# Optimization experiments

Measured on AMD Instinct MI355X. Metric: run time of the kernel, lower is better.

Reference implementation:

```python
import jax, jax.numpy as jnp
import numpy as np

B, T, C = 4, 2048, 1024   # batch, seq (block_size), n_embd
H, D = 16, 64             # num_heads, head_size (H*D == C)


def setup_inputs() -> dict:
    key = jax.random.key(0)
    ks = jax.random.split(key, 6)
    s = 0.02
    return {
        "x":  jax.random.normal(ks[0], (B, T, C), jnp.float32),
        "Wq": jax.random.normal(ks[1], (H, C, D), jnp.float32) * s,
        "Wk": jax.random.normal(ks[2], (H, C, D), jnp.float32) * s,
        "Wv": jax.random.normal(ks[3], (H, C, D), jnp.float32) * s,
        "Wp": jax.random.normal(ks[4], (C, C), jnp.float32) * s,
        "bp": jnp.zeros((C,), jnp.float32),
        "is_masked": 1,
    }


def reference(x, Wq, Wk, Wv, Wp, bp, is_masked):
    # Batched per-head projections (original loops over H separate Linears)
    q = jnp.einsum("btc,hcd->bhtd", x, Wq)
    k = jnp.einsum("btc,hcd->bhtd", x, Wk)
    v = jnp.einsum("btc,hcd->bhtd", x, Wv)
    # NOTE: original divides by sqrt(C) where C = n_embd (input dim), not head_size
    scores = jnp.einsum("bhtd,bhsd->bhts", q, k) / jnp.sqrt(jnp.asarray(C, x.dtype))
    if is_masked:
        causal = jnp.tril(jnp.ones((T, T), bool))
        scores = jnp.where(causal, scores, jnp.asarray(-jnp.inf, scores.dtype))
    attn = jax.nn.softmax(scores, axis=-1)   # dropout is identity in eval mode
    out = jnp.einsum("bhts,bhsd->bhtd", attn, v)
    # concat heads along the last dim: [B,T,H*D] == [B,T,C]
    out = out.transpose(0, 2, 1, 3).reshape(B, T, C)
    return out @ Wp.T + bp
```

## Files before the change

### kernel.cpp

```cpp
#include <hip/hip_runtime.h>
#include <stdint.h>
#include <type_traits>

typedef unsigned short u16;
typedef unsigned int u32;
typedef __attribute__((ext_vector_type(8))) short frag8;
typedef __attribute__((ext_vector_type(4))) float fx4;
typedef __attribute__((ext_vector_type(16))) float fx16;

#define MFMA(a, b, c) __builtin_amdgcn_mfma_f32_16x16x32_bf16((a), (b), (c), 0, 0, 0)
#define MFMA32(a, b, c) __builtin_amdgcn_mfma_f32_32x32x16_bf16((a), (b), (c), 0, 0, 0)

__device__ __forceinline__ void gload16(const void* g, void* l) {
  __builtin_amdgcn_global_load_lds((const __attribute__((address_space(1))) void*)g,
                                   (__attribute__((address_space(3))) void*)l, 16, 0, 0);
}

__device__ __forceinline__ u16 f2bf(float f) {
  union { float f; unsigned int u; } c; c.f = f;
  unsigned int r = c.u + 0x7FFFu + ((c.u >> 16) & 1u);
  return (u16)(r >> 16);
}

__device__ __forceinline__ u32 cvtpk(float lo, float hi) {
  u32 r;
  asm("v_cvt_pk_bf16_f32 %0, %1, %2" : "=v"(r) : "v"(lo), "v"(hi));
  return r;
}

__device__ __forceinline__ float fmax3(float a, float b, float c) {
  return fmaxf(fmaxf(a, b), c);
}


__global__ __launch_bounds__(256) void cvt_x(const float* __restrict__ x, u16* __restrict__ xb) {
  const int n4 = (8192 * 1024) / 4;
  for (int i = blockIdx.x * 256 + threadIdx.x; i < n4; i += 2048 * 256) {
    float4 v = ((const float4*)x)[i];
    ushort4 o;
    o.x = f2bf(v.x); o.y = f2bf(v.y); o.z = f2bf(v.z); o.w = f2bf(v.w);
    ((ushort4*)xb)[i] = o;
  }
}

__global__ __launch_bounds__(256) void cvt_wqkv(const float* __restrict__ Wq,
                                                const float* __restrict__ Wk,
                                                const float* __restrict__ Wv,
                                                u16* __restrict__ Wt) {
  __shared__ u16 Tls[64][72];
  int hh = blockIdx.x;
  int c0 = blockIdx.y * 64;
  int type = hh >> 4, h = hh & 15;
  const float* Wsrc = (type == 0 ? Wq : (type == 1 ? Wk : Wv)) + (size_t)h * 1024 * 64;
  int t = threadIdx.x;
  int cr = t >> 4, q4 = (t & 15) * 4;
  for (int i = 0; i < 4; ++i) {
    int c = cr + i * 16;
    float4 v = *(const float4*)(Wsrc + (size_t)(c0 + c) * 64 + q4);
    Tls[q4 + 0][c] = f2bf(v.x);
    Tls[q4 + 1][c] = f2bf(v.y);
    Tls[q4 + 2][c] = f2bf(v.z);
    Tls[q4 + 3][c] = f2bf(v.w);
  }
  __syncthreads();
  for (int i = 0; i < 4; ++i) {
    int d = cr + i * 16;
    ushort4 o;
    o.x = Tls[d][q4 + 0]; o.y = Tls[d][q4 + 1]; o.z = Tls[d][q4 + 2]; o.w = Tls[d][q4 + 3];
    *(ushort4*)(Wt + ((size_t)hh * 64 + d) * 1024 + c0 + q4) = o;
  }
}

__global__ __launch_bounds__(256) void cvt_wp(const float* __restrict__ Wp, u16* __restrict__ wb) {
  const int n4 = (1024 * 1024) / 4;
  for (int i = blockIdx.x * 256 + threadIdx.x; i < n4; i += 1024 * 256) {
    float4 v = ((const float4*)Wp)[i];
    ushort4 o;
    o.x = f2bf(v.x); o.y = f2bf(v.y); o.z = f2bf(v.z); o.w = f2bf(v.w);
    ((ushort4*)wb)[i] = o;
  }
}

__global__ __launch_bounds__(256) void transpose_v(const u16* __restrict__ Vb, u16* __restrict__ VTg) {
  __shared__ u16 T[64 * 64];
  int bh = blockIdx.x, t0 = blockIdx.y * 64;
  const u16* src = Vb + ((size_t)bh * 2048 + t0) * 64;
  int tid = threadIdx.x;
  int tl = tid >> 2, c16 = (tid & 3) * 16;
  int swzw = (tl & 7) << 4;
  frag8 a = *(const frag8*)(src + (size_t)tl * 64 + c16);
  frag8 b = *(const frag8*)(src + (size_t)tl * 64 + c16 + 8);
  *(frag8*)((char*)T + tl * 128 + ((c16 * 2) ^ swzw)) = a;
  *(frag8*)((char*)T + tl * 128 + ((c16 * 2 + 16) ^ swzw)) = b;
  __syncthreads();
  int d_ = tid & 63;
#pragma unroll
  for (int k = 0; k < 2; ++k) {
    int c_ = (tid >> 6) + 4 * k;
    frag8 o;
#pragma unroll
    for (int j = 0; j < 8; ++j) {
      int t = c_ * 8 + j;
      o[j] = *(const u16*)((const char*)T + t * 128 + ((2 * d_) ^ ((t & 7) << 4)));
    }
    *(frag8*)(VTg + ((size_t)bh * 64 + d_) * 2048 + t0 + c_ * 8) = o;
  }
}


template <int BN, int MODE>
__global__ __launch_bounds__(512, 1) void gemm2(const u16* __restrict__ A, const u16* __restrict__ Bw,
                                                u16* __restrict__ Qb, u16* __restrict__ Kb,
                                                u16* __restrict__ Vb, float* __restrict__ outp,
                                                const float* __restrict__ bp) {
  constexpr int NI = BN / 32;
  constexpr int NB = BN / 64;
  constexpr int BBYTES = BN * 128;
  __shared__ __align__(16) char LDSC[65536 + 3 * BBYTES];
  const int tid = threadIdx.x, w = tid >> 6, lane = tid & 63;
  const int lr = lane & 15, lg = lane >> 4;
  constexpr int NBY = (BN == 192) ? 16 : 8;
  const int wg = blockIdx.x;
  const int xcd = wg & 7, loc = wg >> 3;
  const int bx = xcd * 4 + loc / NBY;
  const int by = loc % NBY;
  const int m0 = bx * 256, n0 = by * BN;
  const int r8 = lane >> 3;
  const int c8 = ((lane & 7) ^ r8) * 8;
  const u16* aS[4];
  const u16* bS[3];
#pragma unroll
  for (int l = 0; l < 4; ++l) aS[l] = A + (size_t)(m0 + l * 64 + w * 8 + r8) * 1024 + c8;
#pragma unroll
  for (int l = 0; l < NB; ++l) bS[l] = Bw + (size_t)(n0 + l * 64 + w * 8 + r8) * 1024 + c8;
  const int wmB = (w >> 1) * 64, wnB = (w & 1) * (BN / 2);

  auto rdA = [&](const char* ab, int mi, int ks) -> frag8 {
    int row = wmB + mi * 16 + lr;
    return *(const frag8*)(ab + row * 128 + ((((ks << 2) + lg) ^ (lr & 7)) << 4));
  };
  auto rdB = [&](const char* bbuf, int ni, int ks) -> frag8 {
    int row = wnB + ni * 16 + lr;
    return *(const frag8*)(bbuf + row * 128 + ((((ks << 2) + lg) ^ (lr & 7)) << 4));
  };

  fx4 acc[4][NI] = {};

#pragma unroll
  for (int l = 0; l < 4; ++l) gload16(aS[l], LDSC + l * 8192 + w * 1024);
#pragma unroll
  for (int l = 0; l < NB; ++l) gload16(bS[l], LDSC + 65536 + l * 8192 + w * 1024);
#pragma unroll
  for (int l = 0; l < NB; ++l) gload16(bS[l] + 64, LDSC + 65536 + BBYTES + l * 8192 + w * 1024);
  if constexpr (NB == 3) asm volatile("s_waitcnt vmcnt(3)" ::: "memory");
  else asm volatile("s_waitcnt vmcnt(2)" ::: "memory");
  __builtin_amdgcn_s_barrier();

  for (int t = 0; t < 16; ++t) {
    const char* ab = LDSC + (t & 1) * 32768;
    const char* bb = LDSC + 65536 + (t % 3) * BBYTES;
    char* abN = LDSC + ((t + 1) & 1) * 32768;
    char* bbN = LDSC + 65536 + ((t + 2) % 3) * BBYTES;
    if (t + 1 < 16) {
#pragma unroll
      for (int l = 0; l < 4; ++l) gload16(aS[l] + (t + 1) * 64, abN + l * 8192 + w * 1024);
    }
    if (t + 2 < 16) {
#pragma unroll
      for (int l = 0; l < NB; ++l) gload16(bS[l] + (t + 2) * 64, bbN + l * 8192 + w * 1024);
    }
    frag8 Bf[NI][2];
#pragma unroll
    for (int ni = 0; ni < NI; ++ni) {
      Bf[ni][0] = rdB(bb, ni, 0);
      Bf[ni][1] = rdB(bb, ni, 1);
    }
    frag8 a0 = rdA(ab, 0, 0), a1 = rdA(ab, 0, 1);
#pragma unroll
    for (int mi = 0; mi < 4; ++mi) {
      frag8 c0 = a0, c1 = a1;
      if (mi < 3) {
        a0 = rdA(ab, mi + 1, 0);
        a1 = rdA(ab, mi + 1, 1);
      }
      __builtin_amdgcn_s_setprio(1);
#pragma unroll
      for (int ni = 0; ni < NI; ++ni) {
        acc[mi][ni] = MFMA(c0, Bf[ni][0], acc[mi][ni]);
        acc[mi][ni] = MFMA(c1, Bf[ni][1], acc[mi][ni]);
      }
      __builtin_amdgcn_s_setprio(0);
    }
    if (t < 14) {
      if constexpr (NB == 3) asm volatile("s_waitcnt vmcnt(3)" ::: "memory");
      else asm volatile("s_waitcnt vmcnt(2)" ::: "memory");
    } else {
      asm volatile("s_waitcnt vmcnt(0)" ::: "memory");
    }
    __builtin_amdgcn_s_barrier();
  }

#pragma unroll
  for (int mi = 0; mi < 4; ++mi)
#pragma unroll
    for (int r = 0; r < 4; ++r) {
      int m = m0 + wmB + mi * 16 + lg * 4 + r;
      if (MODE == 0) {
        int b = m >> 11, tt = m & 2047;
#pragma unroll
        for (int ni = 0; ni < NI; ++ni) {
          int n = n0 + wnB + ni * 16 + lr;
          int type = n >> 10, h = (n >> 6) & 15, d = n & 63;
          u16* dst = (type == 0) ? Qb : ((type == 1) ? Kb : Vb);
          float v = acc[mi][ni][r];
          if (type == 0) v *= 0.04508422002778011f;
          dst[((size_t)(b * 16 + h) * 2048 + tt) * 64 + d] = f2bf(v);
        }
      } else {
#pragma unroll
        for (int ni = 0; ni < NI; ++ni) {
          int n = n0 + wnB + ni * 16 + lr;
          outp[(size_t)m * 1024 + n] = acc[mi][ni][r] + bp[n];
        }
      }
    }
}


__global__ __launch_bounds__(256, 4) void attn(const u16* __restrict__ Qb, const u16* __restrict__ Kb,
                                               const u16* __restrict__ VTg, u16* __restrict__ Ao,
                                               const int* __restrict__ mflag) {
  __shared__ __align__(16) char LDS[32768];
  const int tid = threadIdx.x, w = tid >> 6, lane = tid & 63;
  const int l31 = lane & 31, hi = lane >> 5;
  const int bh = blockIdx.x;
  const int qt = 15 - (int)blockIdx.y;
  const int masked = mflag[0];
  const int qbase = qt * 128;
  const u16* Qh = Qb + (size_t)bh * (2048 * 64);
  const u16* Kh = Kb + (size_t)bh * (2048 * 64);
  const u16* Vh = VTg + (size_t)bh * (64 * 2048);
  const int qrow = qbase + w * 32 + l31;
  frag8 qf[4];
#pragma unroll
  for (int s = 0; s < 4; ++s) qf[s] = *(const frag8*)(Qh + (size_t)qrow * 64 + s * 16 + hi * 8);
  const int srow = lane >> 3;
  const int schunk = ((lane & 7) ^ srow) * 8;
  const int c0 = w * 2, c1 = w * 2 + 1;
  const u16* kg0 = Kh + (size_t)(c0 * 8 + srow) * 64 + schunk;
  const u16* kg1 = Kh + (size_t)(c1 * 8 + srow) * 64 + schunk;
  const u16* vg0 = Vh + (size_t)(c0 * 8 + srow) * 2048 + schunk;
  const u16* vg1 = Vh + (size_t)(c1 * 8 + srow) * 2048 + schunk;
  const int aK = l31 * 128 + ((hi * 16) ^ ((l31 & 7) << 4));
  const int qmax_w = qbase + w * 32 + 31;
  const int qmin_w = qbase + w * 32;
  float m_run = -__builtin_inff(), l_run = 0.f;
  fx16 oa0 = {}, oa1 = {};
  const int nt = masked ? (2 * qt + 2) : 32;

  auto STAGE = [&](int B, int T) {
    size_t ko = (size_t)T * 4096, vo = (size_t)T * 64;
    gload16(kg0 + ko, LDS + B * 8192 + c0 * 1024);
    gload16(kg1 + ko, LDS + B * 8192 + c1 * 1024);
    gload16(vg0 + vo, LDS + 16384 + B * 8192 + c0 * 1024);
    gload16(vg1 + vo, LDS + 16384 + B * 8192 + c1 * 1024);
  };

  auto TILE = [&](auto Bc, int T) {
    constexpr int B = decltype(Bc)::value;
    if (T + 1 < nt) STAGE(B ^ 1, T + 1);
    bool act = (!masked) || (T * 64 <= qmax_w);
    if (act) {
      fx16 s0v = {}, s1v = {};
#pragma unroll
      for (int ds = 0; ds < 4; ++ds) {
        frag8 k0 = *(const frag8*)(LDS + B * 8192 + (aK ^ (ds << 5)));
        frag8 k1 = *(const frag8*)(LDS + B * 8192 + 4096 + (aK ^ (ds << 5)));
        s0v = MFMA32(k0, qf[ds], s0v);
        s1v = MFMA32(k1, qf[ds], s1v);
      }
      if (masked && T * 64 + 63 > qmin_w) {
#pragma unroll
        for (int g = 0; g < 4; ++g)
#pragma unroll
          for (int r = 0; r < 4; ++r) {
            int sg = T * 64 + r + 8 * g + 4 * hi;
            if (sg > qrow) s0v[4 * g + r] = -__builtin_inff();
            if (sg + 32 > qrow) s1v[4 * g + r] = -__builtin_inff();
          }
      }
      float tmx[8];
#pragma unroll
      for (int i = 0; i < 8; ++i)
        tmx[i] = fmaxf(fmaxf(s0v[i], s0v[i + 8]), fmaxf(s1v[i], s1v[i + 8]));
      float r0 = fmax3(tmx[0], tmx[1], tmx[2]);
      float r1 = fmax3(tmx[3], tmx[4], tmx[5]);
      float r2 = fmax3(tmx[6], tmx[7], r0);
      float mx = fmaxf(r1, r2);
      mx = fmaxf(mx, __int_as_float(__shfl_xor(__float_as_int(mx), 32)));
      if (!__all(mx <= m_run + 8.0f)) {
        float mn = fmaxf(m_run, mx);
        float al = __builtin_amdgcn_exp2f(m_run - mn);
#pragma unroll
        for (int i = 0; i < 16; ++i) { oa0[i] *= al; oa1[i] *= al; }
        l_run *= al;
        m_run = mn;
      }
#pragma unroll
      for (int i = 0; i < 16; ++i) s0v[i] = __builtin_amdgcn_exp2f(s0v[i] - m_run);
#pragma unroll
      for (int i = 0; i < 16; ++i) s1v[i] = __builtin_amdgcn_exp2f(s1v[i] - m_run);
      float tps[8];
#pragma unroll
      for (int i = 0; i < 8; ++i)
        tps[i] = (s0v[i] + s0v[i + 8]) + (s1v[i] + s1v[i + 8]);
      float u0 = (tps[0] + tps[1]) + (tps[2] + tps[3]);
      float u1 = (tps[4] + tps[5]) + (tps[6] + tps[7]);
      float ps = u0 + u1;
      ps += __int_as_float(__shfl_xor(__float_as_int(ps), 32));
      l_run += ps;
#pragma unroll
      for (int kt = 0; kt < 4; ++kt) {
        const int b8 = (kt & 1) * 8;
        float p0, p1, p2, p3, p4, p5, p6, p7;
        if (kt < 2) { p0=s0v[b8+0];p1=s0v[b8+1];p2=s0v[b8+2];p3=s0v[b8+3];p4=s0v[b8+4];p5=s0v[b8+5];p6=s0v[b8+6];p7=s0v[b8+7]; }
        else        { p0=s1v[b8+0];p1=s1v[b8+1];p2=s1v[b8+2];p3=s1v[b8+3];p4=s1v[b8+4];p5=s1v[b8+5];p6=s1v[b8+6];p7=s1v[b8+7]; }
        u32 X0 = cvtpk(p0, p1), X1 = cvtpk(p2, p3);
        u32 Y0 = cvtpk(p4, p5), Y1 = cvtpk(p6, p7);
        u32 sel0 = hi ? X0 : Y0, sel1 = hi ? X1 : Y1;
        u32 got0 = (u32)__shfl_xor((int)sel0, 32);
        u32 got1 = (u32)__shfl_xor((int)sel1, 32);
        union { u32 u[4]; frag8 f; } pf;
        pf.u[0] = hi ? got0 : X0;
        pf.u[1] = hi ? got1 : X1;
        pf.u[2] = hi ? Y0 : got0;
        pf.u[3] = hi ? Y1 : got1;
        frag8 v0 = *(const frag8*)(LDS + 16384 + B * 8192 + (aK ^ (kt << 5)));
        frag8 v1 = *(const frag8*)(LDS + 16384 + B * 8192 + 4096 + (aK ^ (kt << 5)));
        oa0 = MFMA32(v0, pf.f, oa0);
        oa1 = MFMA32(v1, pf.f, oa1);
      }
    }
    asm volatile("s_waitcnt vmcnt(0)" ::: "memory");
    __builtin_amdgcn_s_barrier();
  };

  STAGE(0, 0);
  asm volatile("s_waitcnt vmcnt(0)" ::: "memory");
  __builtin_amdgcn_s_barrier();
  int t = 0;
  while (true) {
    TILE(std::integral_constant<int, 0>{}, t); ++t; if (t >= nt) break;
    TILE(std::integral_constant<int, 1>{}, t); ++t; if (t >= nt) break;
  }

  float inv = 1.0f / l_run;
  int b = bh >> 4, hh = bh & 15;
  u16* orow = Ao + ((size_t)b * 2048 + qrow) * 1024 + hh * 64;
#pragma unroll
  for (int g = 0; g < 4; ++g) {
    int d0 = 8 * g + 4 * hi;
    u32 wA = cvtpk(oa0[4 * g + 0] * inv, oa0[4 * g + 1] * inv);
    u32 wB = cvtpk(oa0[4 * g + 2] * inv, oa0[4 * g + 3] * inv);
    u32 wC = cvtpk(oa1[4 * g + 0] * inv, oa1[4 * g + 1] * inv);
    u32 wD = cvtpk(oa1[4 * g + 2] * inv, oa1[4 * g + 3] * inv);
    *(u32*)(orow + d0 + 0) = wA;
    *(u32*)(orow + d0 + 2) = wB;
    *(u32*)(orow + d0 + 32) = wC;
    *(u32*)(orow + d0 + 34) = wD;
  }
}


extern "C" void kernel_launch(void* const* d_in, const int* in_sizes, int n_in,
                              void* d_out, int out_size, void* d_ws, size_t ws_size,
                              hipStream_t stream) {
  const float* x = (const float*)d_in[0];
  const float* Wq = (const float*)d_in[1];
  const float* Wk = (const float*)d_in[2];
  const float* Wv = (const float*)d_in[3];
  const float* Wp = (const float*)d_in[4];
  const float* bp = (const float*)d_in[5];
  const int* is_masked = (const int*)d_in[6];
  float* out = (float*)d_out;
  char* ws = (char*)d_ws;
  u16* Xbf = (u16*)(ws + 0);
  u16* Wt  = (u16*)(ws + 16777216);
  u16* Wpb = (u16*)(ws + 23068672);
  u16* Qb  = (u16*)(ws + 25165824);
  u16* Kb  = (u16*)(ws + 41943040);
  u16* Vb  = (u16*)(ws + 58720256);
  u16* Ao  = (u16*)(ws + 75497472);
  u16* VTg = Xbf;

  cvt_x<<<2048, 256, 0, stream>>>(x, Xbf);
  cvt_wqkv<<<dim3(48, 16), 256, 0, stream>>>(Wq, Wk, Wv, Wt);
  cvt_wp<<<1024, 256, 0, stream>>>(Wp, Wpb);
  gemm2<192, 0><<<512, 512, 0, stream>>>(Xbf, Wt, Qb, Kb, Vb, nullptr, nullptr);
  transpose_v<<<dim3(64, 32), 256, 0, stream>>>(Vb, VTg);
  attn<<<dim3(64, 16), 256, 0, stream>>>(Qb, Kb, VTg, Ao, is_masked);
  gemm2<128, 1><<<256, 512, 0, stream>>>(Ao, Wpb, nullptr, nullptr, nullptr, out, bp);
}
```

Before: 162.4 us.

## Restructure GEMM mainloop into barrier-phased MFMA pairs and shrink attention query tiles

The GEMM mainloop now preloads all A fragments and computes output columns in pairs, with barrier-separated phases, explicit lgkmcnt waits and sched_barriers, and B-tile prefetches spread across the phases. Launch bounds are raised to two blocks per SM. The attention kernel moves from 128-row query tiles with 4 waves to 64-row tiles with 2 waves, doubling the grid and dropping the per-wave causal skip check. The aim is better load/MFMA interleaving and better causal load balance, at the cost of extra barriers and more K/V traffic per query row.

After: 174.1 us. 1.07x slower.

```diff
diff --git a/kernel.cpp b/kernel.cpp
--- a/kernel.cpp
+++ b/kernel.cpp
@@ -109,11 +109,12 @@
 
 
 template <int BN, int MODE>
-__global__ __launch_bounds__(512, 1) void gemm2(const u16* __restrict__ A, const u16* __restrict__ Bw,
+__global__ __launch_bounds__(512, 2) void gemm2(const u16* __restrict__ A, const u16* __restrict__ Bw,
                                                 u16* __restrict__ Qb, u16* __restrict__ Kb,
                                                 u16* __restrict__ Vb, float* __restrict__ outp,
                                                 const float* __restrict__ bp) {
   constexpr int NI = BN / 32;
+  constexpr int NPAIR = NI / 2;
   constexpr int NB = BN / 64;
   constexpr int BBYTES = BN * 128;
   __shared__ __align__(16) char LDSC[65536 + 3 * BBYTES];
@@ -156,48 +157,77 @@
   else asm volatile("s_waitcnt vmcnt(2)" ::: "memory");
   __builtin_amdgcn_s_barrier();
 
+  int bcur = 0;
   for (int t = 0; t < 16; ++t) {
     const char* ab = LDSC + (t & 1) * 32768;
-    const char* bb = LDSC + 65536 + (t % 3) * BBYTES;
+    const char* bb = LDSC + 65536 + bcur * BBYTES;
     char* abN = LDSC + ((t + 1) & 1) * 32768;
-    char* bbN = LDSC + 65536 + ((t + 2) % 3) * BBYTES;
+    int bn2 = bcur + 2; if (bn2 >= 3) bn2 -= 3;
+    char* bbN = LDSC + 65536 + bn2 * BBYTES;
+
+    frag8 Af[4][2];
+#pragma unroll
+    for (int mi = 0; mi < 4; ++mi) {
+      Af[mi][0] = rdA(ab, mi, 0);
+      Af[mi][1] = rdA(ab, mi, 1);
+    }
+    frag8 Bf[2][2];
+    Bf[0][0] = rdB(bb, 0, 0); Bf[0][1] = rdB(bb, 0, 1);
+    Bf[1][0] = rdB(bb, 1, 0); Bf[1][1] = rdB(bb, 1, 1);
     if (t + 1 < 16) {
 #pragma unroll
       for (int l = 0; l < 4; ++l) gload16(aS[l] + (t + 1) * 64, abN + l * 8192 + w * 1024);
     }
-    if (t + 2 < 16) {
-#pragma unroll
-      for (int l = 0; l < NB; ++l) gload16(bS[l] + (t + 2) * 64, bbN + l * 8192 + w * 1024);
-    }
-    frag8 Bf[NI][2];
-#pragma unroll
-    for (int ni = 0; ni < NI; ++ni) {
-      Bf[ni][0] = rdB(bb, ni, 0);
-      Bf[ni][1] = rdB(bb, ni, 1);
-    }
-    frag8 a0 = rdA(ab, 0, 0), a1 = rdA(ab, 0, 1);
-#pragma unroll
-    for (int mi = 0; mi < 4; ++mi) {
-      frag8 c0 = a0, c1 = a1;
-      if (mi < 3) {
-        a0 = rdA(ab, mi + 1, 0);
-        a1 = rdA(ab, mi + 1, 1);
-      }
+    __builtin_amdgcn_s_barrier();
+    asm volatile("s_waitcnt lgkmcnt(0)" ::: "memory");
+    __builtin_amdgcn_sched_barrier(0);
+    __builtin_amdgcn_s_setprio(1);
+#pragma unroll
+    for (int mi = 0; mi < 4; ++mi)
+#pragma unroll
+      for (int ks = 0; ks < 2; ++ks) {
+        acc[mi][0] = MFMA(Af[mi][ks], Bf[0][ks], acc[mi][0]);
+        acc[mi][1] = MFMA(Af[mi][ks], Bf[1][ks], acc[mi][1]);
+      }
+    __builtin_amdgcn_s_setprio(0);
+    __builtin_amdgcn_s_barrier();
+
+#pragma unroll
+    for (int p = 1; p < NPAIR; ++p) {
+      frag8 Bp[2][2];
+      Bp[0][0] = rdB(bb, 2 * p + 0, 0); Bp[0][1] = rdB(bb, 2 * p + 0, 1);
+      Bp[1][0] = rdB(bb, 2 * p + 1, 0); Bp[1][1] = rdB(bb, 2 * p + 1, 1);
+      if (t + 2 < 16) {
+        if (p == 1) {
+          gload16(bS[0] + (t + 2) * 64, bbN + 0 * 8192 + w * 1024);
+          if (NB > 2 || NPAIR == 2) gload16(bS[1] + (t + 2) * 64, bbN + 1 * 8192 + w * 1024);
+        }
+        if (NPAIR == 3 && p == 2 && NB == 3)
+          gload16(bS[2] + (t + 2) * 64, bbN + 2 * 8192 + w * 1024);
+      }
+      __builtin_amdgcn_s_barrier();
+      asm volatile("s_waitcnt lgkmcnt(0)" ::: "memory");
+      __builtin_amdgcn_sched_barrier(0);
       __builtin_amdgcn_s_setprio(1);
 #pragma unroll
-      for (int ni = 0; ni < NI; ++ni) {
-        acc[mi][ni] = MFMA(c0, Bf[ni][0], acc[mi][ni]);
-        acc[mi][ni] = MFMA(c1, Bf[ni][1], acc[mi][ni]);
-      }
+      for (int mi = 0; mi < 4; ++mi)
+#pragma unroll
+        for (int ks = 0; ks < 2; ++ks) {
+          acc[mi][2 * p + 0] = MFMA(Af[mi][ks], Bp[0][ks], acc[mi][2 * p + 0]);
+          acc[mi][2 * p + 1] = MFMA(Af[mi][ks], Bp[1][ks], acc[mi][2 * p + 1]);
+        }
       __builtin_amdgcn_s_setprio(0);
-    }
-    if (t < 14) {
-      if constexpr (NB == 3) asm volatile("s_waitcnt vmcnt(3)" ::: "memory");
-      else asm volatile("s_waitcnt vmcnt(2)" ::: "memory");
-    } else {
-      asm volatile("s_waitcnt vmcnt(0)" ::: "memory");
-    }
-    __builtin_amdgcn_s_barrier();
+      if (p == NPAIR - 1) {
+        if (t < 14) {
+          if constexpr (NB == 3) asm volatile("s_waitcnt vmcnt(3)" ::: "memory");
+          else asm volatile("s_waitcnt vmcnt(2)" ::: "memory");
+        } else {
+          asm volatile("s_waitcnt vmcnt(0)" ::: "memory");
+        }
+      }
+      __builtin_amdgcn_s_barrier();
+    }
+    bcur += 1; if (bcur == 3) bcur = 0;
   }
 
 #pragma unroll
@@ -227,16 +257,16 @@
 }
 
 
-__global__ __launch_bounds__(256, 4) void attn(const u16* __restrict__ Qb, const u16* __restrict__ Kb,
+__global__ __launch_bounds__(128, 4) void attn(const u16* __restrict__ Qb, const u16* __restrict__ Kb,
                                                const u16* __restrict__ VTg, u16* __restrict__ Ao,
                                                const int* __restrict__ mflag) {
   __shared__ __align__(16) char LDS[32768];
   const int tid = threadIdx.x, w = tid >> 6, lane = tid & 63;
   const int l31 = lane & 31, hi = lane >> 5;
   const int bh = blockIdx.x;
-  const int qt = 15 - (int)blockIdx.y;
+  const int qt = 31 - (int)blockIdx.y;
   const int masked = mflag[0];
-  const int qbase = qt * 128;
+  const int qbase = qt * 64;
   const u16* Qh = Qb + (size_t)bh * (2048 * 64);
   const u16* Kh = Kb + (size_t)bh * (2048 * 64);
   const u16* Vh = VTg + (size_t)bh * (64 * 2048);
@@ -246,31 +276,32 @@
   for (int s = 0; s < 4; ++s) qf[s] = *(const frag8*)(Qh + (size_t)qrow * 64 + s * 16 + hi * 8);
   const int srow = lane >> 3;
   const int schunk = ((lane & 7) ^ srow) * 8;
-  const int c0 = w * 2, c1 = w * 2 + 1;
-  const u16* kg0 = Kh + (size_t)(c0 * 8 + srow) * 64 + schunk;
-  const u16* kg1 = Kh + (size_t)(c1 * 8 + srow) * 64 + schunk;
-  const u16* vg0 = Vh + (size_t)(c0 * 8 + srow) * 2048 + schunk;
-  const u16* vg1 = Vh + (size_t)(c1 * 8 + srow) * 2048 + schunk;
+  const u16* kg[4]; const u16* vg[4];
+#pragma unroll
+  for (int i = 0; i < 4; ++i) {
+    int c = w * 4 + i;
+    kg[i] = Kh + (size_t)(c * 8 + srow) * 64 + schunk;
+    vg[i] = Vh + (size_t)(c * 8 + srow) * 2048 + schunk;
+  }
   const int aK = l31 * 128 + ((hi * 16) ^ ((l31 & 7) << 4));
-  const int qmax_w = qbase + w * 32 + 31;
-  const int qmin_w = qbase + w * 32;
   float m_run = -__builtin_inff(), l_run = 0.f;
   fx16 oa0 = {}, oa1 = {};
-  const int nt = masked ? (2 * qt + 2) : 32;
+  const int nt = masked ? (qt + 1) : 32;
 
   auto STAGE = [&](int B, int T) {
     size_t ko = (size_t)T * 4096, vo = (size_t)T * 64;
-    gload16(kg0 + ko, LDS + B * 8192 + c0 * 1024);
-    gload16(kg1 + ko, LDS + B * 8192 + c1 * 1024);
-    gload16(vg0 + vo, LDS + 16384 + B * 8192 + c0 * 1024);
-    gload16(vg1 + vo, LDS + 16384 + B * 8192 + c1 * 1024);
+#pragma unroll
+    for (int i = 0; i < 4; ++i) {
+      int c = w * 4 + i;
+      gload16(kg[i] + ko, LDS + B * 8192 + c * 1024);
+      gload16(vg[i] + vo, LDS + 16384 + B * 8192 + c * 1024);
+    }
   };
 
   auto TILE = [&](auto Bc, int T) {
     constexpr int B = decltype(Bc)::value;
     if (T + 1 < nt) STAGE(B ^ 1, T + 1);
-    bool act = (!masked) || (T * 64 <= qmax_w);
-    if (act) {
+    {
       fx16 s0v = {}, s1v = {};
 #pragma unroll
       for (int ds = 0; ds < 4; ++ds) {
@@ -279,7 +310,7 @@
         s0v = MFMA32(k0, qf[ds], s0v);
         s1v = MFMA32(k1, qf[ds], s1v);
       }
-      if (masked && T * 64 + 63 > qmin_w) {
+      if (masked && T == qt) {
 #pragma unroll
         for (int g = 0; g < 4; ++g)
 #pragma unroll
@@ -398,6 +429,6 @@
   cvt_wp<<<1024, 256, 0, stream>>>(Wp, Wpb);
   gemm2<192, 0><<<512, 512, 0, stream>>>(Xbf, Wt, Qb, Kb, Vb, nullptr, nullptr);
   transpose_v<<<dim3(64, 32), 256, 0, stream>>>(Vb, VTg);
-  attn<<<dim3(64, 16), 256, 0, stream>>>(Qb, Kb, VTg, Ao, is_masked);
+  attn<<<dim3(64, 32), 128, 0, stream>>>(Qb, Kb, VTg, Ao, is_masked);
   gemm2<128, 1><<<256, 512, 0, stream>>>(Ao, Wpb, nullptr, nullptr, nullptr, out, bp);
 }
```
